# Kernel optimization log

Hardware: AMD Instinct MI355X
Metric: run time of the kernel (lower is better)

## Reference

```python
import jax, jax.numpy as jnp
import numpy as np

NEG_INF = -9e15


def setup_inputs() -> dict:
    key = jax.random.key(0)
    k1, k2, k3, k4 = jax.random.split(key, 4)
    N, F_in, H, F_out = 4096, 512, 8, 64
    node_features = jax.random.normal(k1, (N, F_in), dtype=jnp.float32)
    adj_matrix = jax.random.randint(k2, (N, N), 0, 2, dtype=jnp.int32)
    # ensure self-loops so every row has at least one unmasked entry
    adj_matrix = jnp.maximum(adj_matrix, jnp.eye(N, dtype=jnp.int32))
    W = jax.random.normal(k3, (H, F_in, F_out), dtype=jnp.float32) * 0.05
    a = jax.random.normal(k4, (H, 2 * F_out), dtype=jnp.float32) * 0.05
    return {"node_features": node_features, "adj_matrix": adj_matrix, "W": W, "a": a}


def reference(node_features, adj_matrix, W, a):
    alpha = 0.2
    H, F_in, F_out = W.shape
    # Per-head linear projection: [H, N, F_out]
    Wh = jnp.einsum("nf,hfo->hno", node_features, W)
    # Attention logits e_ij = LeakyReLU(a1 . Wh_i + a2 . Wh_j)
    f_src = jnp.einsum("hno,ho->hn", Wh, a[:, :F_out])   # [H, N]
    f_dst = jnp.einsum("hno,ho->hn", Wh, a[:, F_out:])   # [H, N]
    e = jax.nn.leaky_relu(f_src[:, :, None] + f_dst[:, None, :], negative_slope=alpha)  # [H, N, N]
    # Mask by adjacency, softmax over neighbors
    masked = jnp.where(adj_matrix[None, :, :] > 0, e, NEG_INF)
    attn = jax.nn.softmax(masked, axis=-1)               # [H, N, N]
    # Aggregate neighbor features per head
    h_prime = jnp.einsum("hnm,hmo->hno", attn, Wh)       # [H, N, F_out]
    # Concat heads along feature dim -> [N, H*F_out]
    return jnp.transpose(h_prime, (1, 0, 2)).reshape(h_prime.shape[1], H * F_out)
```

## Files before the change

### kernel.cpp

```cpp
#include <hip/hip_runtime.h>
#include <stdint.h>


#define NN 4096
#define FIN 512
#define NH 8
#define FO 64

typedef _Float16 f16x8 __attribute__((ext_vector_type(8)));
typedef _Float16 f16x2 __attribute__((ext_vector_type(2)));
typedef __attribute__((ext_vector_type(4))) float f32x4;

union H8 { f16x8 v; f16x2 p[4]; unsigned u[4]; };
union U2 { unsigned u; f16x2 v; };

__device__ __forceinline__ unsigned short f2h(float f) {
  _Float16 h = (_Float16)f;
  return __builtin_bit_cast(unsigned short, h);
}

__device__ __forceinline__ f16x8 ld_cvt8(const float* p) {
  float4 a = *(const float4*)p, b = *(const float4*)(p + 4);
  f16x8 r;
  r[0] = (_Float16)a.x; r[1] = (_Float16)a.y; r[2] = (_Float16)a.z; r[3] = (_Float16)a.w;
  r[4] = (_Float16)b.x; r[5] = (_Float16)b.y; r[6] = (_Float16)b.z; r[7] = (_Float16)b.w;
  return r;
}

__global__ __launch_bounds__(256) void prep_w_kernel(
    const float* __restrict__ W, const float* __restrict__ a,
    unsigned short* __restrict__ WbT, unsigned short* __restrict__ WAh) {
  int bid = blockIdx.x, tid = threadIdx.x;
  if (bid < 1024) {
    int item = bid * 256 + tid;
    int o = item & 63, k = (item >> 6) & 511, h = item >> 15;
    WbT[h * 32768 + o * 512 + k] = f2h(W[h * 32768 + k * 64 + o]);
  } else {
    int item = (bid - 1024) * 256 + tid;
    int h = item >> 10, which = (item >> 9) & 1, k = item & 511;
    const float4* wp = (const float4*)(W + ((size_t)h * FIN + k) * FO);
    const float4* ap = (const float4*)(a + h * 128 + which * 64);
    float s = 0.f;
#pragma unroll
    for (int o4 = 0; o4 < 16; ++o4) {
      float4 w4 = wp[o4], a4 = ap[o4];
      s += w4.x * a4.x + w4.y * a4.y + w4.z * a4.z + w4.w * a4.w;
    }
    WAh[(h * 2 + which) * FIN + k] = f2h(s);
  }
}

__global__ __launch_bounds__(512, 4) void proj_adj_kernel(
    const float* __restrict__ X, const int* __restrict__ adj,
    const unsigned short* __restrict__ WbT, const unsigned short* __restrict__ WAh,
    unsigned short* __restrict__ Whfrag, float* __restrict__ Rf,
    unsigned short* __restrict__ E1h, unsigned short* __restrict__ E2h,
    unsigned* __restrict__ adjbits) {
  __shared__ float red[4 * 64 * 20];
  int lane = threadIdx.x & 63, wave = threadIdx.x >> 6;
  int row16 = lane & 15, grp = lane >> 4;
  int bx = blockIdx.x;
  if (bx >= 544) {
    int item = (bx - 544) * 512 + threadIdx.x;
    int r = item >> 7, jt = item & 127;
    const int4* p = (const int4*)(adj + (size_t)r * NN + jt * 32);
    unsigned bits = 0;
#pragma unroll
    for (int b = 0; b < 8; ++b) {
      int4 v = p[b];
      bits |= (unsigned)(v.x & 1) << (4 * b);
      bits |= (unsigned)(v.y & 1) << (4 * b + 1);
      bits |= (unsigned)(v.z & 1) << (4 * b + 2);
      bits |= (unsigned)(v.w & 1) << (4 * b + 3);
    }
    adjbits[item] = bits;
    return;
  }
  if (bx >= 512) {
    int i0 = ((bx - 512) * 8 + wave) * 16;
    if (i0 >= NN) return;
    f32x4 acc = {0, 0, 0, 0};
    const float* xb = X + (size_t)(i0 + row16) * FIN + grp * 8;
    const unsigned short* wb = WAh + row16 * FIN + grp * 8;
#pragma unroll
    for (int k0 = 0; k0 < FIN; k0 += 32)
      acc = __builtin_amdgcn_mfma_f32_16x16x32_f16(ld_cvt8(xb + k0),
                                                   *(const f16x8*)(wb + k0), acc, 0, 0, 0);
    int hh = row16 >> 1;
#pragma unroll
    for (int reg = 0; reg < 4; ++reg) {
      int rr = i0 + grp * 4 + reg;
      float v = acc[reg];
      if (row16 & 1) {
        E1h[hh * NN + rr] = f2h(0.5f * __expf(v));
        E2h[hh * NN + rr] = f2h(0.5f * __expf(0.2f * v));
      } else {
        Rf[hh * NN + rr] = __expf(-0.8f * v);
      }
    }
    return;
  }
  int kh = wave >> 2, jb = wave & 3;
  int job = bx * 4 + jb;
  int h = job & 7, rt = job >> 3;
  int i0 = rt * 16;
  f32x4 acc[4] = {{0,0,0,0},{0,0,0,0},{0,0,0,0},{0,0,0,0}};
  const float* xb = X + (size_t)(i0 + row16) * FIN + kh * 256 + grp * 8;
  const unsigned short* wb = WbT + h * (FO * FIN) + row16 * FIN + kh * 256 + grp * 8;
#pragma unroll
  for (int k0 = 0; k0 < 256; k0 += 32) {
    f16x8 af = ld_cvt8(xb + k0);
#pragma unroll
    for (int cb = 0; cb < 4; ++cb)
      acc[cb] = __builtin_amdgcn_mfma_f32_16x16x32_f16(
          af, *(const f16x8*)(wb + cb * 16 * FIN + k0), acc[cb], 0, 0, 0);
  }
  if (kh == 1) {
    float* q = red + (jb * 64 + lane) * 20;
#pragma unroll
    for (int cb = 0; cb < 4; ++cb) *(f32x4*)(q + cb * 4) = acc[cb];
  }
  __syncthreads();
  if (kh == 0) {
    const float* q = red + (jb * 64 + lane) * 20;
#pragma unroll
    for (int cb = 0; cb < 4; ++cb) acc[cb] += *(const f32x4*)(q + cb * 4);
    int jt = i0 >> 5;
    int kk0 = (i0 & 31) + grp * 4;
    int tl = (kk0 >> 3) * 16 + row16;
    int e0 = kk0 & 7;
#pragma unroll
    for (int cb = 0; cb < 4; ++cb) {
      ushort4 pk;
      pk.x = f2h(acc[cb][0]); pk.y = f2h(acc[cb][1]);
      pk.z = f2h(acc[cb][2]); pk.w = f2h(acc[cb][3]);
      *(ushort4*)(Whfrag + (((size_t)h * 128 + jt) * 4 + cb) * 512 + tl * 8 + e0) = pk;
    }
  }
}

struct Tile {
  f16x8 b0, b1, b2, b3;
  f16x8 e1, e2;
};

#define ROWW 132

__global__ __launch_bounds__(256, 2) void gat_kernel(
    const unsigned* __restrict__ adjbits, const unsigned short* __restrict__ Whfrag,
    const float* __restrict__ Rf, const unsigned short* __restrict__ E1h,
    const unsigned short* __restrict__ E2h, float* __restrict__ out) {
  __shared__ __align__(16) char lds[64 * ROWW * 4];
  unsigned* la = (unsigned*)lds;
  int h = blockIdx.y;
  int lane = threadIdx.x & 63, jseg = threadIdx.x >> 6;
  int row16 = lane & 15, grp = lane >> 4;
  int r0 = blockIdx.x * 64;
  int jt0 = jseg * 32;

  {
    int row = threadIdx.x >> 2, seg = threadIdx.x & 3;
    const uint4* src = (const uint4*)(adjbits + (size_t)(r0 + row) * 128 + seg * 32);
    uint4* dst = (uint4*)(la + row * ROWW + seg * 32);
#pragma unroll
    for (int i = 0; i < 8; ++i) dst[i] = src[i];
  }

  f16x2 Rh[4];
#pragma unroll
  for (int gi = 0; gi < 4; ++gi) {
    _Float16 rv = (_Float16)Rf[h * NN + r0 + gi * 16 + row16];
    Rh[gi][0] = rv; Rh[gi][1] = rv;
  }

  H8 ones;
#pragma unroll
  for (int k = 0; k < 4; ++k) ones.u[k] = 0x3C003C00u;

  const unsigned short* wsrc = Whfrag + (size_t)h * 262144 + (size_t)jt0 * 2048 + lane * 8;
  const unsigned short* e1p = E1h + h * NN + jt0 * 32 + grp * 8;
  const unsigned short* e2p = E2h + h * NN + jt0 * 32 + grp * 8;

  f32x4 acc[4][5];
#pragma unroll
  for (int gi = 0; gi < 4; ++gi)
#pragma unroll
    for (int cc = 0; cc < 5; ++cc) acc[gi][cc] = (f32x4){0, 0, 0, 0};

  __syncthreads();

  auto ld = [&](int p, Tile& t) {
    const unsigned short* bs = wsrc + (size_t)p * 2048;
    t.b0 = *(const f16x8*)(bs);
    t.b1 = *(const f16x8*)(bs + 512);
    t.b2 = *(const f16x8*)(bs + 1024);
    t.b3 = *(const f16x8*)(bs + 1536);
    t.e1 = *(const f16x8*)(e1p + p * 32);
    t.e2 = *(const f16x8*)(e2p + p * 32);
  };

  auto compute = [&](int p, const Tile& t) {
    H8 e1, e2;
    e1.v = t.e1; e2.v = t.e2;
    int jt = jt0 + p;
#pragma unroll
    for (int gi = 0; gi < 4; ++gi) {
      unsigned bw = la[(gi * 16 + row16) * ROWW + jt];
      unsigned bb = (bw >> (grp * 8)) & 0xffu;
      unsigned tt = bb | (bb << 15);
      H8 af;
#pragma unroll
      for (int k = 0; k < 4; ++k) {
        f16x2 mx = __builtin_elementwise_max(e1.p[k], Rh[gi] * e2.p[k]);
        U2 m;
        m.u = (tt << (14 - 2 * k)) & 0x40004000u;
        af.p[k] = mx * m.v;
      }
      acc[gi][0] = __builtin_amdgcn_mfma_f32_16x16x32_f16(af.v, t.b0, acc[gi][0], 0, 0, 0);
      acc[gi][1] = __builtin_amdgcn_mfma_f32_16x16x32_f16(af.v, t.b1, acc[gi][1], 0, 0, 0);
      acc[gi][2] = __builtin_amdgcn_mfma_f32_16x16x32_f16(af.v, t.b2, acc[gi][2], 0, 0, 0);
      acc[gi][3] = __builtin_amdgcn_mfma_f32_16x16x32_f16(af.v, t.b3, acc[gi][3], 0, 0, 0);
      acc[gi][4] = __builtin_amdgcn_mfma_f32_16x16x32_f16(af.v, ones.v, acc[gi][4], 0, 0, 0);
    }
  };

  Tile tA, tB;
  ld(0, tA);
#pragma unroll 1
  for (int p2 = 0; p2 < 15; ++p2) {
    ld(2 * p2 + 1, tB);
    asm volatile("" ::: "memory");
    compute(2 * p2, tA);
    ld(2 * p2 + 2, tA);
    asm volatile("" ::: "memory");
    compute(2 * p2 + 1, tB);
  }
  ld(31, tB);
  compute(30, tA);
  compute(31, tB);

  __syncthreads();
  float* red = (float*)lds;
#pragma unroll
  for (int cc = 0; cc < 5; ++cc) {
    if (jseg != 0) {
#pragma unroll
      for (int gi = 0; gi < 4; ++gi)
        *(f32x4*)(red + (((jseg - 1) * 4 + gi) * 64 + lane) * 4) = acc[gi][cc];
    }
    __syncthreads();
    if (jseg == 0) {
#pragma unroll
      for (int s = 0; s < 3; ++s)
#pragma unroll
        for (int gi = 0; gi < 4; ++gi)
          acc[gi][cc] += *(const f32x4*)(red + ((s * 4 + gi) * 64 + lane) * 4);
    }
    __syncthreads();
  }

  if (jseg == 0) {
#pragma unroll
    for (int gi = 0; gi < 4; ++gi) {
#pragma unroll
      for (int reg = 0; reg < 4; ++reg) {
        float inv = 1.0f / acc[gi][4][reg];
        int row = r0 + gi * 16 + grp * 4 + reg;
        float* op = out + (size_t)row * (NH * FO) + h * FO + row16;
        op[0]  = acc[gi][0][reg] * inv;
        op[16] = acc[gi][1][reg] * inv;
        op[32] = acc[gi][2][reg] * inv;
        op[48] = acc[gi][3][reg] * inv;
      }
    }
  }
}

extern "C" void kernel_launch(void* const* d_in, const int* in_sizes, int n_in,
                              void* d_out, int out_size, void* d_ws, size_t ws_size,
                              hipStream_t stream) {
  const float* X  = (const float*)d_in[0];
  const int* adj  = (const int*)d_in[1];
  const float* W  = (const float*)d_in[2];
  const float* a  = (const float*)d_in[3];
  float* out = (float*)d_out;
  char* ws = (char*)d_ws;

  unsigned short* WbT    = (unsigned short*)(ws + 0);
  unsigned* adjbits      = (unsigned*)(ws + 524288);
  unsigned short* Whfrag = (unsigned short*)(ws + 2621440);
  unsigned short* WAh    = (unsigned short*)(ws + 6815744);
  float* Rf              = (float*)(ws + 6832128);
  unsigned short* E1h    = (unsigned short*)(ws + 6963200);
  unsigned short* E2h    = (unsigned short*)(ws + 7028736);

  prep_w_kernel<<<1056, 256, 0, stream>>>(W, a, WbT, WAh);
  proj_adj_kernel<<<1568, 512, 0, stream>>>(X, adj, WbT, WAh, Whfrag, Rf, E1h, E2h,
                                            adjbits);
  gat_kernel<<<dim3(64, 8), 256, 0, stream>>>(adjbits, Whfrag, Rf, E1h, E2h, out);
}
```

Baseline: 75.75 us.

## Drop split-K LDS reduction in projection, use double-buffered register prefetch

The projection part of proj_adj_kernel no longer splits K across two wave groups and reduces through shared memory with a barrier. Each wave now owns one (head, row-tile) job over the full K=512 and software-pipelines its global loads with two register buffers, keeping the loop rolled. This halves the projection block count and removes the LDS traffic and __syncthreads, but gives each wave a longer serial loop and more live registers.

```diff
diff --git a/kernel.cpp b/kernel.cpp
--- a/kernel.cpp
+++ b/kernel.cpp
@@ -19,12 +19,14 @@
   return __builtin_bit_cast(unsigned short, h);
 }
 
-__device__ __forceinline__ f16x8 ld_cvt8(const float* p) {
-  float4 a = *(const float4*)p, b = *(const float4*)(p + 4);
+__device__ __forceinline__ f16x8 cvt8(float4 a, float4 b) {
   f16x8 r;
   r[0] = (_Float16)a.x; r[1] = (_Float16)a.y; r[2] = (_Float16)a.z; r[3] = (_Float16)a.w;
   r[4] = (_Float16)b.x; r[5] = (_Float16)b.y; r[6] = (_Float16)b.z; r[7] = (_Float16)b.w;
   return r;
+}
+__device__ __forceinline__ f16x8 ld_cvt8(const float* p) {
+  return cvt8(*(const float4*)p, *(const float4*)(p + 4));
 }
 
 __global__ __launch_bounds__(256) void prep_w_kernel(
@@ -56,12 +58,11 @@
     unsigned short* __restrict__ Whfrag, float* __restrict__ Rf,
     unsigned short* __restrict__ E1h, unsigned short* __restrict__ E2h,
     unsigned* __restrict__ adjbits) {
-  __shared__ float red[4 * 64 * 20];
   int lane = threadIdx.x & 63, wave = threadIdx.x >> 6;
   int row16 = lane & 15, grp = lane >> 4;
   int bx = blockIdx.x;
-  if (bx >= 544) {
-    int item = (bx - 544) * 512 + threadIdx.x;
+  if (bx >= 288) {
+    int item = (bx - 288) * 512 + threadIdx.x;
     int r = item >> 7, jt = item & 127;
     const int4* p = (const int4*)(adj + (size_t)r * NN + jt * 32);
     unsigned bits = 0;
@@ -76,8 +77,8 @@
     adjbits[item] = bits;
     return;
   }
-  if (bx >= 512) {
-    int i0 = ((bx - 512) * 8 + wave) * 16;
+  if (bx >= 256) {
+    int i0 = ((bx - 256) * 8 + wave) * 16;
     if (i0 >= NN) return;
     f32x4 acc = {0, 0, 0, 0};
     const float* xb = X + (size_t)(i0 + row16) * FIN + grp * 8;
@@ -100,42 +101,58 @@
     }
     return;
   }
-  int kh = wave >> 2, jb = wave & 3;
-  int job = bx * 4 + jb;
+  int job = bx * 8 + wave;
   int h = job & 7, rt = job >> 3;
   int i0 = rt * 16;
+  const float* xb = X + (size_t)(i0 + row16) * FIN + grp * 8;
+  const unsigned short* wb = WbT + h * (FO * FIN) + row16 * FIN + grp * 8;
   f32x4 acc[4] = {{0,0,0,0},{0,0,0,0},{0,0,0,0},{0,0,0,0}};
-  const float* xb = X + (size_t)(i0 + row16) * FIN + kh * 256 + grp * 8;
-  const unsigned short* wb = WbT + h * (FO * FIN) + row16 * FIN + kh * 256 + grp * 8;
-#pragma unroll
-  for (int k0 = 0; k0 < 256; k0 += 32) {
-    f16x8 af = ld_cvt8(xb + k0);
-#pragma unroll
-    for (int cb = 0; cb < 4; ++cb)
-      acc[cb] = __builtin_amdgcn_mfma_f32_16x16x32_f16(
-          af, *(const f16x8*)(wb + cb * 16 * FIN + k0), acc[cb], 0, 0, 0);
-  }
-  if (kh == 1) {
-    float* q = red + (jb * 64 + lane) * 20;
-#pragma unroll
-    for (int cb = 0; cb < 4; ++cb) *(f32x4*)(q + cb * 4) = acc[cb];
-  }
-  __syncthreads();
-  if (kh == 0) {
-    const float* q = red + (jb * 64 + lane) * 20;
-#pragma unroll
-    for (int cb = 0; cb < 4; ++cb) acc[cb] += *(const f32x4*)(q + cb * 4);
-    int jt = i0 >> 5;
-    int kk0 = (i0 & 31) + grp * 4;
-    int tl = (kk0 >> 3) * 16 + row16;
-    int e0 = kk0 & 7;
-#pragma unroll
-    for (int cb = 0; cb < 4; ++cb) {
-      ushort4 pk;
-      pk.x = f2h(acc[cb][0]); pk.y = f2h(acc[cb][1]);
-      pk.z = f2h(acc[cb][2]); pk.w = f2h(acc[cb][3]);
-      *(ushort4*)(Whfrag + (((size_t)h * 128 + jt) * 4 + cb) * 512 + tl * 8 + e0) = pk;
-    }
+
+  float4 xaA, xbA, xaB, xbB;
+  f16x8 w0A, w1A, w2A, w3A, w0B, w1B, w2B, w3B;
+#define PLD(S, p)                                                     \
+  {                                                                   \
+    xa##S = *(const float4*)(xb + (p) * 32);                          \
+    xb##S = *(const float4*)(xb + (p) * 32 + 4);                      \
+    w0##S = *(const f16x8*)(wb + 0 * 16 * FIN + (p) * 32);            \
+    w1##S = *(const f16x8*)(wb + 1 * 16 * FIN + (p) * 32);            \
+    w2##S = *(const f16x8*)(wb + 2 * 16 * FIN + (p) * 32);            \
+    w3##S = *(const f16x8*)(wb + 3 * 16 * FIN + (p) * 32);            \
+  }
+#define PCMP(S)                                                       \
+  {                                                                   \
+    f16x8 af = cvt8(xa##S, xb##S);                                    \
+    acc[0] = __builtin_amdgcn_mfma_f32_16x16x32_f16(af, w0##S, acc[0], 0, 0, 0); \
+    acc[1] = __builtin_amdgcn_mfma_f32_16x16x32_f16(af, w1##S, acc[1], 0, 0, 0); \
+    acc[2] = __builtin_amdgcn_mfma_f32_16x16x32_f16(af, w2##S, acc[2], 0, 0, 0); \
+    acc[3] = __builtin_amdgcn_mfma_f32_16x16x32_f16(af, w3##S, acc[3], 0, 0, 0); \
+  }
+  PLD(A, 0)
+#pragma unroll 1
+  for (int p2 = 0; p2 < 7; ++p2) {
+    PLD(B, 2 * p2 + 1)
+    asm volatile("" ::: "memory");
+    PCMP(A)
+    PLD(A, 2 * p2 + 2)
+    asm volatile("" ::: "memory");
+    PCMP(B)
+  }
+  PLD(B, 15)
+  asm volatile("" ::: "memory");
+  PCMP(A)
+  PCMP(B)
+#undef PLD
+#undef PCMP
+  int jt = i0 >> 5;
+  int kk0 = (i0 & 31) + grp * 4;
+  int tl = (kk0 >> 3) * 16 + row16;
+  int e0 = kk0 & 7;
+#pragma unroll
+  for (int cb = 0; cb < 4; ++cb) {
+    ushort4 pk;
+    pk.x = f2h(acc[cb][0]); pk.y = f2h(acc[cb][1]);
+    pk.z = f2h(acc[cb][2]); pk.w = f2h(acc[cb][3]);
+    *(ushort4*)(Whfrag + (((size_t)h * 128 + jt) * 4 + cb) * 512 + tl * 8 + e0) = pk;
   }
 }
 
@@ -295,7 +312,7 @@
   unsigned short* E2h    = (unsigned short*)(ws + 7028736);
 
   prep_w_kernel<<<1056, 256, 0, stream>>>(W, a, WbT, WAh);
-  proj_adj_kernel<<<1568, 512, 0, stream>>>(X, adj, WbT, WAh, Whfrag, Rf, E1h, E2h,
+  proj_adj_kernel<<<1312, 512, 0, stream>>>(X, adj, WbT, WAh, Whfrag, Rf, E1h, E2h,
                                             adjbits);
   gat_kernel<<<dim3(64, 8), 256, 0, stream>>>(adjbits, Whfrag, Rf, E1h, E2h, out);
 }
```

New measurement: 76.87 us. Within noise of the previous version (+1.5%).

## Pre-convert X to fp16 in prep kernel and loop adjacency packing over fewer blocks

Applied to the files above, without the earlier changes.

X is converted to fp16 once in the prep kernel (2048 extra blocks), so the projection MFMA paths load f16x8 directly instead of reading and converting fp32 twice. The adjacency bit-packing blocks now each handle four chunks in a loop, cutting the proj grid from 1568 to 800 blocks. The shared buffer is enlarged and retyped, though it appears unused beyond the old reduction. The trade-off is an extra 4 MB fp16 write and read of X through the workspace.

```diff
diff --git a/kernel.cpp b/kernel.cpp
--- a/kernel.cpp
+++ b/kernel.cpp
@@ -19,23 +19,16 @@
   return __builtin_bit_cast(unsigned short, h);
 }
 
-__device__ __forceinline__ f16x8 ld_cvt8(const float* p) {
-  float4 a = *(const float4*)p, b = *(const float4*)(p + 4);
-  f16x8 r;
-  r[0] = (_Float16)a.x; r[1] = (_Float16)a.y; r[2] = (_Float16)a.z; r[3] = (_Float16)a.w;
-  r[4] = (_Float16)b.x; r[5] = (_Float16)b.y; r[6] = (_Float16)b.z; r[7] = (_Float16)b.w;
-  return r;
-}
-
 __global__ __launch_bounds__(256) void prep_w_kernel(
-    const float* __restrict__ W, const float* __restrict__ a,
-    unsigned short* __restrict__ WbT, unsigned short* __restrict__ WAh) {
+    const float* __restrict__ W, const float* __restrict__ a, const float* __restrict__ X,
+    unsigned short* __restrict__ WbT, unsigned short* __restrict__ WAh,
+    unsigned short* __restrict__ Xh) {
   int bid = blockIdx.x, tid = threadIdx.x;
   if (bid < 1024) {
     int item = bid * 256 + tid;
     int o = item & 63, k = (item >> 6) & 511, h = item >> 15;
     WbT[h * 32768 + o * 512 + k] = f2h(W[h * 32768 + k * 64 + o]);
-  } else {
+  } else if (bid < 1056) {
     int item = (bid - 1024) * 256 + tid;
     int h = item >> 10, which = (item >> 9) & 1, k = item & 511;
     const float4* wp = (const float4*)(W + ((size_t)h * FIN + k) * FO);
@@ -47,44 +40,52 @@
       s += w4.x * a4.x + w4.y * a4.y + w4.z * a4.z + w4.w * a4.w;
     }
     WAh[(h * 2 + which) * FIN + k] = f2h(s);
+  } else {
+    int item = (bid - 1056) * 256 + tid;
+    float4 v = ((const float4*)X)[item];
+    ushort4 o;
+    o.x = f2h(v.x); o.y = f2h(v.y); o.z = f2h(v.z); o.w = f2h(v.w);
+    ((ushort4*)Xh)[item] = o;
   }
 }
 
 __global__ __launch_bounds__(512, 4) void proj_adj_kernel(
-    const float* __restrict__ X, const int* __restrict__ adj,
+    const unsigned short* __restrict__ Xh, const int* __restrict__ adj,
     const unsigned short* __restrict__ WbT, const unsigned short* __restrict__ WAh,
     unsigned short* __restrict__ Whfrag, float* __restrict__ Rf,
     unsigned short* __restrict__ E1h, unsigned short* __restrict__ E2h,
     unsigned* __restrict__ adjbits) {
-  __shared__ float red[4 * 64 * 20];
+  __shared__ __align__(16) char lmem[33792];
   int lane = threadIdx.x & 63, wave = threadIdx.x >> 6;
   int row16 = lane & 15, grp = lane >> 4;
   int bx = blockIdx.x;
   if (bx >= 544) {
-    int item = (bx - 544) * 512 + threadIdx.x;
-    int r = item >> 7, jt = item & 127;
-    const int4* p = (const int4*)(adj + (size_t)r * NN + jt * 32);
-    unsigned bits = 0;
-#pragma unroll
-    for (int b = 0; b < 8; ++b) {
-      int4 v = p[b];
-      bits |= (unsigned)(v.x & 1) << (4 * b);
-      bits |= (unsigned)(v.y & 1) << (4 * b + 1);
-      bits |= (unsigned)(v.z & 1) << (4 * b + 2);
-      bits |= (unsigned)(v.w & 1) << (4 * b + 3);
-    }
-    adjbits[item] = bits;
+#pragma unroll 1
+    for (int c = 0; c < 4; ++c) {
+      int item = ((bx - 544) + c * 256) * 512 + threadIdx.x;
+      const int4* p = (const int4*)(adj + (size_t)item * 32);
+      unsigned bits = 0;
+#pragma unroll
+      for (int b = 0; b < 8; ++b) {
+        int4 v = p[b];
+        bits |= (unsigned)(v.x & 1) << (4 * b);
+        bits |= (unsigned)(v.y & 1) << (4 * b + 1);
+        bits |= (unsigned)(v.z & 1) << (4 * b + 2);
+        bits |= (unsigned)(v.w & 1) << (4 * b + 3);
+      }
+      adjbits[item] = bits;
+    }
     return;
   }
   if (bx >= 512) {
     int i0 = ((bx - 512) * 8 + wave) * 16;
     if (i0 >= NN) return;
     f32x4 acc = {0, 0, 0, 0};
-    const float* xb = X + (size_t)(i0 + row16) * FIN + grp * 8;
+    const unsigned short* xb = Xh + (size_t)(i0 + row16) * FIN + grp * 8;
     const unsigned short* wb = WAh + row16 * FIN + grp * 8;
 #pragma unroll
     for (int k0 = 0; k0 < FIN; k0 += 32)
-      acc = __builtin_amdgcn_mfma_f32_16x16x32_f16(ld_cvt8(xb + k0),
+      acc = __builtin_amdgcn_mfma_f32_16x16x32_f16(*(const f16x8*)(xb + k0),
                                                    *(const f16x8*)(wb + k0), acc, 0, 0, 0);
     int hh = row16 >> 1;
 #pragma unroll
@@ -100,16 +101,17 @@
     }
     return;
   }
+  float* red = (float*)lmem;
   int kh = wave >> 2, jb = wave & 3;
   int job = bx * 4 + jb;
   int h = job & 7, rt = job >> 3;
   int i0 = rt * 16;
   f32x4 acc[4] = {{0,0,0,0},{0,0,0,0},{0,0,0,0},{0,0,0,0}};
-  const float* xb = X + (size_t)(i0 + row16) * FIN + kh * 256 + grp * 8;
+  const unsigned short* xb = Xh + (size_t)(i0 + row16) * FIN + kh * 256 + grp * 8;
   const unsigned short* wb = WbT + h * (FO * FIN) + row16 * FIN + kh * 256 + grp * 8;
 #pragma unroll
   for (int k0 = 0; k0 < 256; k0 += 32) {
-    f16x8 af = ld_cvt8(xb + k0);
+    f16x8 af = *(const f16x8*)(xb + k0);
 #pragma unroll
     for (int cb = 0; cb < 4; ++cb)
       acc[cb] = __builtin_amdgcn_mfma_f32_16x16x32_f16(
@@ -293,9 +295,10 @@
   float* Rf              = (float*)(ws + 6832128);
   unsigned short* E1h    = (unsigned short*)(ws + 6963200);
   unsigned short* E2h    = (unsigned short*)(ws + 7028736);
-
-  prep_w_kernel<<<1056, 256, 0, stream>>>(W, a, WbT, WAh);
-  proj_adj_kernel<<<1568, 512, 0, stream>>>(X, adj, WbT, WAh, Whfrag, Rf, E1h, E2h,
-                                            adjbits);
+  unsigned short* Xh     = (unsigned short*)(ws + 7094272);
+
+  prep_w_kernel<<<3104, 256, 0, stream>>>(W, a, X, WbT, WAh, Xh);
+  proj_adj_kernel<<<800, 512, 0, stream>>>(Xh, adj, WbT, WAh, Whfrag, Rf, E1h, E2h,
+                                           adjbits);
   gat_kernel<<<dim3(64, 8), 256, 0, stream>>>(adjbits, Whfrag, Rf, E1h, E2h, out);
 }
```

Measured after the change: 75.62 us. Within noise of the previous version (-0.2%).
